# Performance work log

Hardware: AMD Instinct MI355X
Metric: run time of the kernel (lower is better)

Reference implementation:

```python
import jax, jax.numpy as jnp
import numpy as np

N, IN_F, OUT_F, H = 4096, 256, 512, 8
D = OUT_F // H  # hidden per head
NEG_SLOPE = 0.2


def setup_inputs() -> dict:
    key = jax.random.key(0)
    k1, k2, k3 = jax.random.split(key, 3)
    inp = jax.random.normal(k1, (N, IN_F), dtype=jnp.float32)
    A = jnp.zeros((N, N), dtype=jnp.float32)  # additive adjacency mask
    # xavier_uniform for W [out, in]
    limW = float(np.sqrt(6.0 / (IN_F + H * D)))
    W = jax.random.uniform(k2, (H * D, IN_F), minval=-limW, maxval=limW, dtype=jnp.float32)
    lima = float(np.sqrt(6.0 / (H * D + 1)))
    a_left = jax.random.uniform(k3, (1, H, D), minval=-lima, maxval=lima, dtype=jnp.float32)
    return {"inp": inp, "A": A, "W": W, "a_left": a_left}


def reference(inp, A, W, a_left):
    # h: [N, H, D]
    h = (inp @ W.T).reshape(-1, H, D)
    # NOTE: source uses a_left for BOTH source and target scores (a_right is dead code)
    scores = jnp.sum(h * a_left, axis=-1)  # [N, H]
    s = scores.T  # [H, N]
    # [H, N, N] additive attention logits
    logits = jax.nn.leaky_relu(s[:, :, None] + s[:, None, :], negative_slope=NEG_SLOPE)
    logits = logits + A[None, :, :]
    att = jax.nn.softmax(logits, axis=-1)  # [H, N, N]
    # bmm: [H,N,N] x [H,N,D] -> [H,N,D] -> [N,H,D]
    out = jnp.einsum('hij,jhd->ihd', att, h)
    return out.reshape(-1, H * D)
```

## Files before the change

kernel.cpp:

```cpp
#include <hip/hip_runtime.h>
#include <math.h>

#define N 4096
#define IN_F 256
#define OUT_F 512
#define H 8
#define D 64
#define NEG 0.2f
#define JC 1024
#define LOG2E 1.44269504f

typedef __attribute__((ext_vector_type(8))) short bf16x8;
typedef __attribute__((ext_vector_type(4))) float f32x4;

__device__ __forceinline__ float leaky(float x) { return fmaxf(x, NEG * x); }

__device__ __forceinline__ unsigned short f2bf(float x) {
    union { float f; unsigned u; } v; v.f = x;
    unsigned r = v.u + 0x7fff + ((v.u >> 16) & 1);
    return (unsigned short)(r >> 16);
}

__device__ __forceinline__ unsigned fmap(float x) {
    union { float f; unsigned u; } v; v.f = x;
    return (v.u & 0x80000000u) ? ~v.u : (v.u | 0x80000000u);
}
__device__ __forceinline__ float funmap(unsigned m) {
    union { float f; unsigned u; } v;
    v.u = (m & 0x80000000u) ? (m & 0x7fffffffu) : ~m;
    return v.f;
}

__device__ __forceinline__ void dma16(const void* g, void* l) {
    __builtin_amdgcn_global_load_lds((const __attribute__((address_space(1))) void*)g,
                                     (__attribute__((address_space(3))) void*)l, 16, 0, 0);
}

__global__ __launch_bounds__(256) void k_gemm(const float* __restrict__ inp,
                                              const float* __restrict__ W,
                                              const float* __restrict__ a_left,
                                              unsigned short* __restrict__ hbT,
                                              float* __restrict__ s,
                                              unsigned* __restrict__ smaxU) {
    __shared__ float As[64][68];
    __shared__ float Bs[64][68];
    __shared__ unsigned short h_st[64][72];
    __shared__ float s_red[64];

    const int t = threadIdx.x;
    const int bi = blockIdx.x;
    const int head = blockIdx.y;
    const int ty = t >> 4, tx = t & 15;
    const int lr = t >> 2;
    const int cq = (t & 3) * 16;

    float4 pa[4], pb[4];
    auto loadrk = [&](int k0) {
        const float* ip = &inp[(size_t)(bi * 64 + lr) * IN_F + k0 + cq];
        const float* wp = &W[(size_t)(head * 64 + lr) * IN_F + k0 + cq];
#pragma unroll
        for (int q = 0; q < 4; ++q) {
            pa[q] = *(const float4*)&ip[q * 4];
            pb[q] = *(const float4*)&wp[q * 4];
        }
    };
    loadrk(0);

    float acc[4][4] = {};
    for (int k0 = 0; k0 < IN_F; k0 += 64) {
        __syncthreads();
#pragma unroll
        for (int q = 0; q < 4; ++q)
#pragma unroll
            for (int j = 0; j < 4; ++j) {
                As[cq + q * 4 + j][lr] = ((const float*)&pa[q])[j];
                Bs[cq + q * 4 + j][lr] = ((const float*)&pb[q])[j];
            }
        __syncthreads();
        if (k0 + 64 < IN_F) loadrk(k0 + 64);
#pragma unroll
        for (int k = 0; k < 64; ++k) {
            float4 a4 = *(const float4*)&As[k][ty * 4];
            float4 b4 = *(const float4*)&Bs[k][tx * 4];
            float a[4] = {a4.x, a4.y, a4.z, a4.w};
            float b[4] = {b4.x, b4.y, b4.z, b4.w};
#pragma unroll
            for (int r = 0; r < 4; ++r)
#pragma unroll
                for (int c = 0; c < 4; ++c) acc[r][c] = fmaf(a[r], b[c], acc[r][c]);
        }
    }

    float aL[4];
#pragma unroll
    for (int c = 0; c < 4; ++c) aL[c] = a_left[head * D + tx * 4 + c];
#pragma unroll
    for (int r = 0; r < 4; ++r) {
        float sp = acc[r][0] * aL[0] + acc[r][1] * aL[1] + acc[r][2] * aL[2] + acc[r][3] * aL[3];
        sp += __shfl_xor(sp, 1); sp += __shfl_xor(sp, 2);
        sp += __shfl_xor(sp, 4); sp += __shfl_xor(sp, 8);
        if (tx == 0) {
            s[head * N + bi * 64 + ty * 4 + r] = sp;
            s_red[ty * 4 + r] = sp;
        }
    }
    __syncthreads();
    if (t < 64) {
        float m = s_red[t];
        for (int off = 32; off; off >>= 1) m = fmaxf(m, __shfl_down(m, off, 64));
        if (t == 0) atomicMax(&smaxU[head], fmap(m));
    }

#pragma unroll
    for (int r = 0; r < 4; ++r) {
        ushort4 v;
        v.x = f2bf(acc[r][0]); v.y = f2bf(acc[r][1]);
        v.z = f2bf(acc[r][2]); v.w = f2bf(acc[r][3]);
        *(ushort4*)&h_st[ty * 4 + r][tx * 4] = v;
    }
    __syncthreads();
    {
        const int d = t >> 2, iq = (t & 3) * 16;
        unsigned short us[16];
#pragma unroll
        for (int k = 0; k < 16; ++k) us[k] = h_st[iq + k][d];
        unsigned short* dst = &hbT[((size_t)(head * D + d)) * N + bi * 64 + iq];
#pragma unroll
        for (int q = 0; q < 4; ++q) {
            ushort4 v = {us[q * 4 + 0], us[q * 4 + 1], us[q * 4 + 2], us[q * 4 + 3]};
            *(ushort4*)&dst[q * 4] = v;
        }
    }
}

__global__ __launch_bounds__(256) void k_rowmax(const float* __restrict__ A,
                                                float* __restrict__ rmax) {
    int i = blockIdx.x;
    const float* row = &A[(size_t)i * N];
    float m = -1e30f;
    for (int j = threadIdx.x * 4; j < N; j += 256 * 4) {
        float4 v = *(const float4*)&row[j];
        m = fmaxf(fmaxf(fmaxf(m, v.x), fmaxf(v.y, v.z)), v.w);
    }
    for (int off = 32; off; off >>= 1) m = fmaxf(m, __shfl_down(m, off, 64));
    __shared__ float red[4];
    if ((threadIdx.x & 63) == 0) red[threadIdx.x >> 6] = m;
    __syncthreads();
    if (threadIdx.x == 0) rmax[i] = fmaxf(fmaxf(red[0], red[1]), fmaxf(red[2], red[3]));
}

__global__ __launch_bounds__(512, 2) void k_attn(const float* __restrict__ A,
                                                 const unsigned short* __restrict__ hbT,
                                                 const float* __restrict__ s,
                                                 const unsigned* __restrict__ smaxU,
                                                 const float* __restrict__ rmax,
                                                 float* __restrict__ out,
                                                 float* __restrict__ Z) {
    __shared__ float A_st[2][2048];
    __shared__ unsigned short hT_st[2][16384];
    __shared__ float s_ch[8 * JC];

    const int t = threadIdx.x;
    const int bid = blockIdx.x;
    const int k8 = bid & 7;
    const int jcid = k8 >> 1;
    const int itile = (bid >> 3) + ((k8 & 1) << 5);
    const int i0 = itile * 64;
    const int j0 = jcid * JC;

    const int lane = t & 63, wave = t >> 6;
    const int quad = lane >> 4, li = lane & 15;
    const int wg = wave & 3, hg = wave >> 2;
    const int myrow = i0 + wg * 16 + li;

#pragma unroll
    for (int q = 0; q < 4; ++q) {
        int idx = (q * 512 + t) * 4;
        int hh = idx >> 10;
        int jj = idx & (JC - 1);
        float4 v = *(const float4*)&s[hh * N + j0 + jj];
        v.x *= LOG2E; v.y *= LOG2E; v.z *= LOG2E; v.w *= LOG2E;
        *(float4*)&s_ch[idx] = v;
    }

    const float rmv = rmax[myrow];
    float sI[4], mb[4];
#pragma unroll
    for (int h = 0; h < 4; ++h) {
        int ha = hg * 4 + h;
        float sr = s[ha * N + myrow];
        float sm = funmap(smaxU[ha]);
        float x = sr + sm;
        mb[h] = (leaky(x) + rmv) * LOG2E;
        sI[h] = sr * LOG2E;
    }

    const int ar = t >> 3, ac = t & 7;
    const float* gA = &A[(size_t)(i0 + ar) * N + j0 + ((ac ^ (ar & 7)) * 4)];
    const unsigned short* gH[4];
#pragma unroll
    for (int q = 0; q < 4; ++q) {
        int m = q * 512 + t, R = m >> 2, sl = m & 3;
        gH[q] = &hbT[(size_t)R * N + j0 + ((sl ^ ((R >> 1) & 3)) * 8)];
    }

    dma16(gA, &A_st[0][t * 4]);
#pragma unroll
    for (int q = 0; q < 4; ++q) dma16(gH[q], &hT_st[0][(q * 512 + t) * 8]);
    __syncthreads();

    f32x4 acc[4][4] = {{{0,0,0,0}},{{0,0,0,0}},{{0,0,0,0}},{{0,0,0,0}}};
    float zs[4] = {0.f, 0.f, 0.f, 0.f};

    const int arow = wg * 16 + li;
    const int sw0 = (quad * 2) ^ (arow & 7);
    const int sw1 = (quad * 2 + 1) ^ (arow & 7);
    const int hsw = quad ^ ((li >> 1) & 3);

#pragma unroll 2
    for (int it = 0; it < JC / 32; ++it) {
        const int cur = it & 1;
        if (it + 1 < JC / 32) {
            const int jn = (it + 1) * 32;
            dma16(gA + jn, &A_st[cur ^ 1][t * 4]);
#pragma unroll
            for (int q = 0; q < 4; ++q)
                dma16(gH[q] + jn, &hT_st[cur ^ 1][(q * 512 + t) * 8]);
        }
        const float* bA = A_st[cur];
        const unsigned short* bH = hT_st[cur];
        const int jt = it * 32;

        float4 a0 = *(const float4*)&bA[(arow * 8 + sw0) * 4];
        float4 a1 = *(const float4*)&bA[(arow * 8 + sw1) * 4];
        float av[8] = {a0.x, a0.y, a0.z, a0.w, a1.x, a1.y, a1.z, a1.w};
#pragma unroll
        for (int p = 0; p < 8; ++p) av[p] *= LOG2E;

#pragma unroll
        for (int h = 0; h < 4; ++h) {
            const int ha = hg * 4 + h;
            float4 s0 = *(const float4*)&s_ch[ha * JC + jt + quad * 8];
            float4 s1 = *(const float4*)&s_ch[ha * JC + jt + quad * 8 + 4];
            float sv[8] = {s0.x, s0.y, s0.z, s0.w, s1.x, s1.y, s1.z, s1.w};
            union { bf16x8 v; unsigned u[4]; } P;
#pragma unroll
            for (int p = 0; p < 4; ++p) {
                float x0 = sI[h] + sv[2 * p + 0];
                float x1 = sI[h] + sv[2 * p + 1];
                float w0 = __builtin_amdgcn_exp2f(fmaxf(x0, NEG * x0) - mb[h] + av[2 * p + 0]);
                float w1 = __builtin_amdgcn_exp2f(fmaxf(x1, NEG * x1) - mb[h] + av[2 * p + 1]);
                zs[h] += w0 + w1;
                P.u[p] = ((unsigned)f2bf(w1) << 16) | (unsigned)f2bf(w0);
            }
#pragma unroll
            for (int db = 0; db < 4; ++db) {
                const int R = ha * 64 + db * 16 + li;
                bf16x8 hf = *(const bf16x8*)&bH[(R * 4 + hsw) * 8];
                acc[h][db] = __builtin_amdgcn_mfma_f32_16x16x32_bf16(P.v, hf, acc[h][db], 0, 0, 0);
            }
        }
        __syncthreads();
    }

#pragma unroll
    for (int h = 0; h < 4; ++h) {
        float z = zs[h];
        z += __shfl_xor(z, 16);
        z += __shfl_xor(z, 32);
        if (quad == 0) atomicAdd(&Z[(hg * 4 + h) * N + myrow], z);
    }

#pragma unroll
    for (int h = 0; h < 4; ++h) {
#pragma unroll
        for (int r = 0; r < 4; ++r) {
            float* op = &out[(size_t)(i0 + wg * 16 + quad * 4 + r) * OUT_F + (hg * 4 + h) * D];
#pragma unroll
            for (int db = 0; db < 4; ++db) atomicAdd(&op[db * 16 + li], acc[h][db][r]);
        }
    }
}

__global__ __launch_bounds__(256) void k_norm(float* __restrict__ out,
                                              const float* __restrict__ Z) {
    int idx = blockIdx.x * 256 + threadIdx.x;
    int i = idx >> 9, hd = idx & 511, hh = hd >> 6;
    out[idx] = out[idx] / Z[hh * N + i];
}

extern "C" void kernel_launch(void* const* d_in, const int* in_sizes, int n_in,
                              void* d_out, int out_size, void* d_ws, size_t ws_size,
                              hipStream_t stream) {
    const float* inp = (const float*)d_in[0];
    const float* A = (const float*)d_in[1];
    const float* W = (const float*)d_in[2];
    const float* a_left = (const float*)d_in[3];
    float* out = (float*)d_out;

    unsigned short* hbT = (unsigned short*)d_ws;
    float* s = (float*)((char*)d_ws + (size_t)H * D * N * 2);
    float* Z = s + (size_t)H * N;
    unsigned* smaxU = (unsigned*)(Z + (size_t)H * N);
    float* rmax = (float*)(smaxU + 8);

    hipMemsetAsync(out, 0, (size_t)N * OUT_F * sizeof(float), stream);
    hipMemsetAsync(Z, 0, (size_t)H * N * sizeof(float) + 8 * sizeof(unsigned), stream);

    k_gemm<<<dim3(N / 64, H), 256, 0, stream>>>(inp, W, a_left, hbT, s, smaxU);
    k_rowmax<<<dim3(N), 256, 0, stream>>>(A, rmax);
    k_attn<<<dim3(256), 512, 0, stream>>>(A, hbT, s, smaxU, rmax, out, Z);
    k_norm<<<dim3(N * OUT_F / 256), 256, 0, stream>>>(out, Z);
}
```

Measured before the change: 216.8 us.

## Halve attention j-chunk, load mask from global into registers, raise occupancy

Halves the j-chunk per attention block so the grid doubles to 512 blocks, and raises the launch bound to 4 blocks per CU. The adjacency tile is no longer staged in LDS through async DMA; each thread reads its own mask values straight into registers with a one-step register prefetch. This cuts LDS use and aims for more blocks resident at once. The exp argument is restructured so the mask-minus-max term is computed once per head, bf16 packing moves to the library intrinsic, and the GEMM LDS row pitch is changed from 68 to 69 to alter bank mapping. In exchange, twice as many atomic adds hit the output and Z, and register pressure under the tighter launch bound may cause spills.

```diff
diff --git a/kernel.cpp b/kernel.cpp
--- a/kernel.cpp
+++ b/kernel.cpp
@@ -1,4 +1,5 @@
 #include <hip/hip_runtime.h>
+#include <hip/hip_bf16.h>
 #include <math.h>
 
 #define N 4096
@@ -7,7 +8,8 @@
 #define H 8
 #define D 64
 #define NEG 0.2f
-#define JC 1024
+#define JC 512
+#define NS (JC / 32)
 #define LOG2E 1.44269504f
 
 typedef __attribute__((ext_vector_type(8))) short bf16x8;
@@ -19,6 +21,12 @@
     union { float f; unsigned u; } v; v.f = x;
     unsigned r = v.u + 0x7fff + ((v.u >> 16) & 1);
     return (unsigned short)(r >> 16);
+}
+
+__device__ __forceinline__ unsigned pk_bf16(float a, float b) {
+    __hip_bfloat162 h2 = __float22bfloat162_rn(float2{a, b});
+    union { __hip_bfloat162 h; unsigned u; } u; u.h = h2;
+    return u.u;
 }
 
 __device__ __forceinline__ unsigned fmap(float x) {
@@ -42,8 +50,8 @@
                                               unsigned short* __restrict__ hbT,
                                               float* __restrict__ s,
                                               unsigned* __restrict__ smaxU) {
-    __shared__ float As[64][68];
-    __shared__ float Bs[64][68];
+    __shared__ float As[64][69];
+    __shared__ float Bs[64][69];
     __shared__ unsigned short h_st[64][72];
     __shared__ float s_red[64];
 
@@ -149,22 +157,20 @@
     if (threadIdx.x == 0) rmax[i] = fmaxf(fmaxf(red[0], red[1]), fmaxf(red[2], red[3]));
 }
 
-__global__ __launch_bounds__(512, 2) void k_attn(const float* __restrict__ A,
+__global__ __launch_bounds__(512, 4) void k_attn(const float* __restrict__ A,
                                                  const unsigned short* __restrict__ hbT,
                                                  const float* __restrict__ s,
                                                  const unsigned* __restrict__ smaxU,
                                                  const float* __restrict__ rmax,
                                                  float* __restrict__ out,
                                                  float* __restrict__ Z) {
-    __shared__ float A_st[2][2048];
     __shared__ unsigned short hT_st[2][16384];
-    __shared__ float s_ch[8 * JC];
+    __shared__ float s_ch[H * JC];
 
     const int t = threadIdx.x;
     const int bid = blockIdx.x;
-    const int k8 = bid & 7;
-    const int jcid = k8 >> 1;
-    const int itile = (bid >> 3) + ((k8 & 1) << 5);
+    const int jcid = bid & 7;
+    const int itile = bid >> 3;
     const int i0 = itile * 64;
     const int j0 = jcid * JC;
 
@@ -174,13 +180,13 @@
     const int myrow = i0 + wg * 16 + li;
 
 #pragma unroll
-    for (int q = 0; q < 4; ++q) {
-        int idx = (q * 512 + t) * 4;
-        int hh = idx >> 10;
-        int jj = idx & (JC - 1);
+    for (int q = 0; q < 2; ++q) {
+        int idx4 = q * 512 + t;
+        int hh = idx4 >> 7;
+        int jj = (idx4 * 4) & (JC - 1);
         float4 v = *(const float4*)&s[hh * N + j0 + jj];
         v.x *= LOG2E; v.y *= LOG2E; v.z *= LOG2E; v.w *= LOG2E;
-        *(float4*)&s_ch[idx] = v;
+        *(float4*)&s_ch[idx4 * 4] = v;
     }
 
     const float rmv = rmax[myrow];
@@ -195,8 +201,6 @@
         sI[h] = sr * LOG2E;
     }
 
-    const int ar = t >> 3, ac = t & 7;
-    const float* gA = &A[(size_t)(i0 + ar) * N + j0 + ((ac ^ (ar & 7)) * 4)];
     const unsigned short* gH[4];
 #pragma unroll
     for (int q = 0; q < 4; ++q) {
@@ -204,7 +208,10 @@
         gH[q] = &hbT[(size_t)R * N + j0 + ((sl ^ ((R >> 1) & 3)) * 8)];
     }
 
-    dma16(gA, &A_st[0][t * 4]);
+    const float* Ap = &A[(size_t)myrow * N + j0 + quad * 8];
+    float4 ac0 = *(const float4*)&Ap[0];
+    float4 ac1 = *(const float4*)&Ap[4];
+
 #pragma unroll
     for (int q = 0; q < 4; ++q) dma16(gH[q], &hT_st[0][(q * 512 + t) * 8]);
     __syncthreads();
@@ -212,30 +219,27 @@
     f32x4 acc[4][4] = {{{0,0,0,0}},{{0,0,0,0}},{{0,0,0,0}},{{0,0,0,0}}};
     float zs[4] = {0.f, 0.f, 0.f, 0.f};
 
-    const int arow = wg * 16 + li;
-    const int sw0 = (quad * 2) ^ (arow & 7);
-    const int sw1 = (quad * 2 + 1) ^ (arow & 7);
     const int hsw = quad ^ ((li >> 1) & 3);
 
 #pragma unroll 2
-    for (int it = 0; it < JC / 32; ++it) {
+    for (int it = 0; it < NS; ++it) {
         const int cur = it & 1;
-        if (it + 1 < JC / 32) {
+        const bool more = (it + 1 < NS);
+        float4 an0, an1;
+        if (more) {
             const int jn = (it + 1) * 32;
-            dma16(gA + jn, &A_st[cur ^ 1][t * 4]);
 #pragma unroll
             for (int q = 0; q < 4; ++q)
                 dma16(gH[q] + jn, &hT_st[cur ^ 1][(q * 512 + t) * 8]);
-        }
-        const float* bA = A_st[cur];
+            an0 = *(const float4*)&Ap[jn];
+            an1 = *(const float4*)&Ap[jn + 4];
+        }
         const unsigned short* bH = hT_st[cur];
         const int jt = it * 32;
 
-        float4 a0 = *(const float4*)&bA[(arow * 8 + sw0) * 4];
-        float4 a1 = *(const float4*)&bA[(arow * 8 + sw1) * 4];
-        float av[8] = {a0.x, a0.y, a0.z, a0.w, a1.x, a1.y, a1.z, a1.w};
-#pragma unroll
-        for (int p = 0; p < 8; ++p) av[p] *= LOG2E;
+        float avl[8] = {ac0.x, ac0.y, ac0.z, ac0.w, ac1.x, ac1.y, ac1.z, ac1.w};
+#pragma unroll
+        for (int p = 0; p < 8; ++p) avl[p] *= LOG2E;
 
 #pragma unroll
         for (int h = 0; h < 4; ++h) {
@@ -243,15 +247,18 @@
             float4 s0 = *(const float4*)&s_ch[ha * JC + jt + quad * 8];
             float4 s1 = *(const float4*)&s_ch[ha * JC + jt + quad * 8 + 4];
             float sv[8] = {s0.x, s0.y, s0.z, s0.w, s1.x, s1.y, s1.z, s1.w};
+            float amb[8];
+#pragma unroll
+            for (int p = 0; p < 8; ++p) amb[p] = avl[p] - mb[h];
             union { bf16x8 v; unsigned u[4]; } P;
 #pragma unroll
             for (int p = 0; p < 4; ++p) {
                 float x0 = sI[h] + sv[2 * p + 0];
                 float x1 = sI[h] + sv[2 * p + 1];
-                float w0 = __builtin_amdgcn_exp2f(fmaxf(x0, NEG * x0) - mb[h] + av[2 * p + 0]);
-                float w1 = __builtin_amdgcn_exp2f(fmaxf(x1, NEG * x1) - mb[h] + av[2 * p + 1]);
+                float w0 = __builtin_amdgcn_exp2f(fmaxf(x0, NEG * x0) + amb[2 * p + 0]);
+                float w1 = __builtin_amdgcn_exp2f(fmaxf(x1, NEG * x1) + amb[2 * p + 1]);
                 zs[h] += w0 + w1;
-                P.u[p] = ((unsigned)f2bf(w1) << 16) | (unsigned)f2bf(w0);
+                P.u[p] = pk_bf16(w0, w1);
             }
 #pragma unroll
             for (int db = 0; db < 4; ++db) {
@@ -261,6 +268,7 @@
             }
         }
         __syncthreads();
+        if (more) { ac0 = an0; ac1 = an1; }
     }
 
 #pragma unroll
@@ -309,6 +317,6 @@
 
     k_gemm<<<dim3(N / 64, H), 256, 0, stream>>>(inp, W, a_left, hbT, s, smaxU);
     k_rowmax<<<dim3(N), 256, 0, stream>>>(A, rmax);
-    k_attn<<<dim3(256), 512, 0, stream>>>(A, hbT, s, smaxU, rmax, out, Z);
+    k_attn<<<dim3(64 * (N / JC)), 512, 0, stream>>>(A, hbT, s, smaxU, rmax, out, Z);
     k_norm<<<dim3(N * OUT_F / 256), 256, 0, stream>>>(out, Z);
 }
```

Result: slower. 282.9 us (+30.5%).
